# Kernel optimization log

Measured on AMD Instinct MI355X. Metric: run time of the kernel, lower is better.

## Reference

```python
import jax, jax.numpy as jnp
import numpy as np

NUM_LAYERS = 3


def setup_inputs() -> dict:
    key = jax.random.key(0)
    k1, k2, k3 = jax.random.split(key, 3)
    B, LT, LC, F = 16, 256, 768, 256
    batch_target = jax.random.normal(k1, (B, LT, F), dtype=jnp.float32)
    batch_claim = jax.random.normal(k2, (B, LC, F), dtype=jnp.float32)
    # adjacency is accepted but mathematically unused (original masked_fill is non-in-place and discarded)
    batch_adj = jax.random.randint(jax.random.fold_in(key, 7), (B, LT + LC, LT + LC), 0, 2, dtype=jnp.int32)
    # per-layer trans_linear weights, nn.Linear(F, F, bias=False): y = x @ W.T, W is [out, in]
    W_trans = jax.random.normal(k3, (NUM_LAYERS, F, F), dtype=jnp.float32) * (1.0 / np.sqrt(F))
    return {"batch_target": batch_target, "batch_claim": batch_claim, "batch_adj": batch_adj, "W_trans": W_trans}


def _gcn_layer(node_rep, W):
    # dot attention: score[b,i,j] = <h_i, h_j>  (symmetric all-pairs dot product)
    # NOTE: original's masked_fill(batch_adj == 0, -1e9) is NOT in-place and its
    # result is discarded, so no masking is applied -- reproduced faithfully here.
    corr = jnp.einsum('bif,bjf->bij', node_rep, node_rep)
    attn = jax.nn.softmax(corr, axis=2)              # softmax over j (dim=2)
    trans = jnp.einsum('blf,gf->blg', node_rep, W)   # trans_linear (bias=False)
    node_out = jax.nn.relu(node_rep + jnp.einsum('bij,bjf->bif', attn, trans))
    return node_out, attn


def reference(batch_target, batch_claim, batch_adj, W_trans):
    target_len = batch_target.shape[1]
    node_rep = jnp.concatenate([batch_target, batch_claim], axis=1)  # [B, L, F]
    all_node_rep, all_corr_score = (), ()
    for i in range(NUM_LAYERS):
        node_rep, corr_score = _gcn_layer(node_rep, W_trans[i])
        all_node_rep = all_node_rep + (node_rep,)
        all_corr_score = all_corr_score + (corr_score,)
        # gcn_dropout: identity in eval mode
    target_rep = node_rep[:, :target_len, :]
    claim_rep = node_rep[:, target_len:, :]
    return (target_rep, claim_rep, all_node_rep, all_corr_score)
```

## Files before the change

### kernel.cpp

```cpp
#include <hip/hip_runtime.h>

typedef _Float16 h16;
typedef _Float16 h16x8 __attribute__((ext_vector_type(8)));
typedef _Float16 h16x4 __attribute__((ext_vector_type(4)));
typedef float    f32x4 __attribute__((ext_vector_type(4)));

#define NBATCH 16
#define LROWS  1024
#define FDIM   256

#define OFF_TGT 0ull
#define OFF_CLM 1048576ull
#define OFF_NR  4194304ull
#define OFF_AT  16777216ull

__device__ __forceinline__ void split2(float x, h16& h, h16& l) {
    h = (h16)x;
    l = (h16)(x - (float)h);
}

typedef const __attribute__((address_space(1))) void gvoid;
typedef __attribute__((address_space(3))) void lvoid;
__device__ __forceinline__ void gl_lds16(const void* g, void* l) {
    __builtin_amdgcn_global_load_lds((gvoid*)g, (lvoid*)l, 16, 0, 0);
}

__device__ const unsigned char TRI_I[36] = {
    0,0,0,0,0,0,0,0, 1,1,1,1,1,1,1, 2,2,2,2,2,2, 3,3,3,3,3, 4,4,4,4, 5,5,5, 6,6, 7};
__device__ const unsigned char TRI_J[36] = {
    0,1,2,3,4,5,6,7, 1,2,3,4,5,6,7, 2,3,4,5,6,7, 3,4,5,6,7, 4,5,6,7, 5,6,7, 6,7, 7};

__global__ __launch_bounds__(256) void convert_all(const float* __restrict__ tgt,
                                                   const float* __restrict__ clm,
                                                   const float* __restrict__ W,
                                                   h16* __restrict__ xh, h16* __restrict__ xl,
                                                   h16* __restrict__ wh) {
    int bid = blockIdx.x;
    if (bid < 4096) {
        int b, i;
        if (bid < 2048) { b = bid & 7;       i = bid >> 3; }
        else            { b = 8 + (bid & 7); i = (bid - 2048) >> 3; }
        size_t e = ((size_t)b << 18) + (size_t)i * 1024 + (size_t)threadIdx.x * 4;
        int rf = (int)(e & 262143);
        int r  = rf >> 8, f = rf & 255;
        const float* src = (r < 256)
            ? tgt + ((size_t)b << 16) + ((size_t)r << 8) + f
            : clm + (size_t)b * 196608 + ((size_t)(r - 256) << 8) + f;
        f32x4 v = *(const f32x4*)src;
        h16x4 hv, lv;
#pragma unroll
        for (int j = 0; j < 4; ++j) { h16 hh, ll; split2(v[j], hh, ll); hv[j] = hh; lv[j] = ll; }
        *(h16x4*)(xh + e) = hv;
        *(h16x4*)(xl + e) = lv;
    } else {
        size_t e = ((size_t)(bid - 4096) * 256 + threadIdx.x) * 4;
        f32x4 v = *(const f32x4*)(W + e);
        h16x4 hv;
#pragma unroll
        for (int j = 0; j < 4; ++j) hv[j] = (h16)v[j];
        *(h16x4*)(wh + e) = hv;
    }
}

__global__ __launch_bounds__(256, 3) void gemm_ct(
    const h16* __restrict__ Xh, const h16* __restrict__ Xl,
    const h16* __restrict__ Wh,
    h16* __restrict__ Ptil, float2* __restrict__ part,
    h16* __restrict__ Th) {
    const int b = blockIdx.x & 15;
    const int u = blockIdx.x >> 4;
    const bool isCorr = u < 36;
    int it, jt;
    if (isCorr) { it = TRI_I[u]; jt = TRI_J[u]; }
    else        { int v = u - 36; it = v >> 1; jt = v & 1; }
    const int i0 = it * 128;
    const int j0 = jt * 128;
    const int t  = threadIdx.x;
    const int lane = t & 63, wid = t >> 6;
    const int wr = wid >> 1, wc = wid & 1;

    __shared__ alignas(16) char lds[32768];

    const size_t arow = ((size_t)b * LROWS + i0) * 256;
    const h16* bHp; const h16* bLp; size_t brow;
    if (isCorr) { bHp = Xh; bLp = Xl; brow = ((size_t)b * LROWS + j0) * 256; }
    else        { bHp = Wh; bLp = Xl; brow = (size_t)j0 * 256; }

    f32x4 acc[4][4];
#pragma unroll
    for (int i = 0; i < 4; ++i)
#pragma unroll
        for (int j = 0; j < 4; ++j) acc[i][j] = (f32x4){0.f, 0.f, 0.f, 0.f};

    const int grow = t >> 2;
    const int gq   = t & 3;

    for (int kt = 0; kt < 8; ++kt) {
        __syncthreads();
#pragma unroll
        for (int p = 0; p < 2; ++p) {
            int r = p * 64 + grow;
            size_t so = (size_t)r * 256 + kt * 32 + ((gq ^ ((r >> 1) & 3)) << 3);
            char* d = lds + p * 4096 + wid * 1024;
            gl_lds16(Xh + arow + so, d);
            gl_lds16(Xl + arow + so, d + 8192);
            gl_lds16(bHp + brow + so, d + 16384);
            if (isCorr) gl_lds16(bLp + brow + so, d + 24576);
        }
        __syncthreads();

        const int kq = lane >> 4;
        const int rA = wr * 64 + (lane & 15);
        const int rB = wc * 64 + (lane & 15);
        h16x8 ah[4], al[4], bh[4], bl[4];
#pragma unroll
        for (int mi = 0; mi < 4; ++mi) {
            int r   = rA + mi * 16;
            int off = r * 64 + ((kq ^ ((r >> 1) & 3)) << 4);
            ah[mi] = *(const h16x8*)(lds + off);
            al[mi] = *(const h16x8*)(lds + 8192 + off);
        }
#pragma unroll
        for (int nj = 0; nj < 4; ++nj) {
            int r   = rB + nj * 16;
            int off = r * 64 + ((kq ^ ((r >> 1) & 3)) << 4);
            bh[nj] = *(const h16x8*)(lds + 16384 + off);
            if (isCorr) bl[nj] = *(const h16x8*)(lds + 24576 + off);
        }
        __builtin_amdgcn_s_setprio(1);
#pragma unroll
        for (int mi = 0; mi < 4; ++mi)
#pragma unroll
            for (int nj = 0; nj < 4; ++nj) {
                acc[mi][nj] = __builtin_amdgcn_mfma_f32_16x16x32_f16(ah[mi], bh[nj], acc[mi][nj], 0, 0, 0);
                acc[mi][nj] = __builtin_amdgcn_mfma_f32_16x16x32_f16(al[mi], bh[nj], acc[mi][nj], 0, 0, 0);
                if (isCorr)
                    acc[mi][nj] = __builtin_amdgcn_mfma_f32_16x16x32_f16(ah[mi], bl[nj], acc[mi][nj], 0, 0, 0);
            }
        __builtin_amdgcn_s_setprio(0);
    }

    const int mBase = i0 + wr * 64;
    const int nBase = j0 + wc * 64;
    if (isCorr) {
        h16* Pb = Ptil + (size_t)b * LROWS * 1024;
        {
            const int chunk = jt * 2 + wc;
#pragma unroll
            for (int mi = 0; mi < 4; ++mi)
#pragma unroll
                for (int rg = 0; rg < 4; ++rg) {
                    float v0 = acc[mi][0][rg], v1 = acc[mi][1][rg];
                    float v2 = acc[mi][2][rg], v3 = acc[mi][3][rg];
                    float mx = fmaxf(fmaxf(v0, v1), fmaxf(v2, v3));
#pragma unroll
                    for (int off = 8; off >= 1; off >>= 1) mx = fmaxf(mx, __shfl_xor(mx, off, 64));
                    float e0 = __expf(v0 - mx), e1 = __expf(v1 - mx);
                    float e2 = __expf(v2 - mx), e3 = __expf(v3 - mx);
                    float s = e0 + e1 + e2 + e3;
#pragma unroll
                    for (int off = 8; off >= 1; off >>= 1) s += __shfl_xor(s, off, 64);
                    int row = mBase + mi * 16 + ((lane >> 4) * 4) + rg;
                    if ((lane & 15) == 0)
                        part[((size_t)b * 1024 + row) * 16 + chunk] = make_float2(mx, s);
                    size_t rb = (size_t)row * 1024 + nBase + (lane & 15);
                    Pb[rb]      = (h16)e0;
                    Pb[rb + 16] = (h16)e1;
                    Pb[rb + 32] = (h16)e2;
                    Pb[rb + 48] = (h16)e3;
                }
        }
        if (it != jt) {
            __syncthreads();
            const int chunk = it * 2 + wr;
            const int cl0 = wc * 64 + (lane & 15);
            const int r40 = wr * 64 + ((lane >> 4) << 2);
#pragma unroll
            for (int nj = 0; nj < 4; ++nj) {
                float mx = -3.0e38f;
#pragma unroll
                for (int mi = 0; mi < 4; ++mi)
#pragma unroll
                    for (int rg = 0; rg < 4; ++rg) mx = fmaxf(mx, acc[mi][nj][rg]);
                mx = fmaxf(mx, __shfl_xor(mx, 16, 64));
                mx = fmaxf(mx, __shfl_xor(mx, 32, 64));
                float s = 0.f;
                h16x4 pt[4];
#pragma unroll
                for (int mi = 0; mi < 4; ++mi)
#pragma unroll
                    for (int rg = 0; rg < 4; ++rg) {
                        float e = __expf(acc[mi][nj][rg] - mx);
                        s += e;
                        pt[mi][rg] = (h16)e;
                    }
                s += __shfl_xor(s, 16, 64);
                s += __shfl_xor(s, 32, 64);
                int n = nBase + nj * 16 + (lane & 15);
                if (lane < 16)
                    part[((size_t)b * 1024 + n) * 16 + chunk] = make_float2(mx, s);
                const int cl = cl0 + nj * 16;
#pragma unroll
                for (int mi = 0; mi < 4; ++mi) {
                    int r4 = r40 + mi * 16;
                    *(h16x4*)(lds + cl * 256 + (((r4 ^ ((cl & 7) << 2))) << 1)) = pt[mi];
                }
            }
            __syncthreads();
#pragma unroll
            for (int i8 = 0; i8 < 8; ++i8) {
                int cl = wid * 32 + i8 * 4 + (lane >> 4);
                int R  = (lane & 15) * 8;
                int k4 = (cl & 7) << 2;
                h16x4 v0 = *(const h16x4*)(lds + cl * 256 + (((R    ) ^ k4) << 1));
                h16x4 v1 = *(const h16x4*)(lds + cl * 256 + (((R + 4) ^ k4) << 1));
                h16x8 vv;
                vv[0] = v0[0]; vv[1] = v0[1]; vv[2] = v0[2]; vv[3] = v0[3];
                vv[4] = v1[0]; vv[5] = v1[1]; vv[6] = v1[2]; vv[7] = v1[3];
                *(h16x8*)(Pb + (size_t)(j0 + cl) * 1024 + i0 + R) = vv;
            }
        }
    } else {
#pragma unroll
        for (int mi = 0; mi < 4; ++mi)
#pragma unroll
            for (int nj = 0; nj < 4; ++nj) {
                int n  = nBase + nj * 16 + (lane & 15);
                int m0 = mBase + mi * 16 + ((lane >> 4) * 4);
                h16x4 hv;
#pragma unroll
                for (int rg = 0; rg < 4; ++rg) hv[rg] = (h16)acc[mi][nj][rg];
                size_t off = ((size_t)b * 256 + n) * 1024 + m0;
                *(h16x4*)(Th + off) = hv;
            }
    }
}

__global__ __launch_bounds__(256, 4) void gemm_pv(
    const h16* __restrict__ Ptil, const float2* __restrict__ part,
    float* __restrict__ At,
    const h16* __restrict__ Th,
    h16* __restrict__ Xh, h16* __restrict__ Xl,
    float* __restrict__ NodeOut, float* __restrict__ OutBase, int last) {
    const int id   = blockIdx.x;
    const int b    = (id & 7) | (((id >> 3) & 1) << 3);
    const int mt   = id >> 4;
    const int i0   = mt * 32;
    const int t    = threadIdx.x;
    const int lane = t & 63, wid = t >> 6;
    const int wc   = wid;

    __shared__ alignas(16) char lds[38912];
    float* sc = (float*)(lds + 36864);

    if (t < 32) {
        const float2* pp = part + ((size_t)b * 1024 + i0 + t) * 16;
        float2 v[16];
        float M = -3.0e38f;
#pragma unroll
        for (int c = 0; c < 16; ++c) { v[c] = pp[c]; M = fmaxf(M, v[c].x); }
        float S = 0.f;
#pragma unroll
        for (int c = 0; c < 16; ++c) S += v[c].y * __expf(v[c].x - M);
        float inv = 1.0f / S;
#pragma unroll
        for (int c = 0; c < 16; ++c) sc[t * 16 + c] = __expf(v[c].x - M) * inv;
    }
    __syncthreads();

    const h16* Prow = Ptil + ((size_t)b * LROWS + i0) * 1024;
    float* Arow = At + ((size_t)b * LROWS + i0) * 1024;
    const size_t tbase = (size_t)b * 256 * 1024;

    const int ar = t >> 3;
    const int ac = t & 7;

    f32x4 acc[2][4];
#pragma unroll
    for (int i = 0; i < 2; ++i)
#pragma unroll
        for (int j = 0; j < 4; ++j) acc[i][j] = (f32x4){0.f, 0.f, 0.f, 0.f};

    for (int kt = 0; kt < 16; ++kt) {
        h16x8 pt = *(const h16x8*)(Prow + (size_t)ar * 1024 + kt * 64 + ac * 8);
        float s  = sc[ar * 16 + kt];
        __syncthreads();

#pragma unroll
        for (int itr = 0; itr < 8; ++itr) {
            int g = itr * 32 + ar;
            size_t so = tbase + (size_t)g * 1024 + kt * 64 + ((ac ^ (g & 7)) << 3);
            char* d = lds + 4096 + itr * 4096 + wid * 1024;
            gl_lds16(Th + so, d);
        }

        f32x4 plo, phi;
#pragma unroll
        for (int e = 0; e < 4; ++e) plo[e] = (float)pt[e] * s;
#pragma unroll
        for (int e = 0; e < 4; ++e) phi[e] = (float)pt[4 + e] * s;
        *(f32x4*)(Arow + (size_t)ar * 1024 + kt * 64 + ac * 8)     = plo;
        *(f32x4*)(Arow + (size_t)ar * 1024 + kt * 64 + ac * 8 + 4) = phi;
        h16x8 a16;
#pragma unroll
        for (int e = 0; e < 4; ++e) { a16[e] = (h16)plo[e]; a16[4 + e] = (h16)phi[e]; }
        *(h16x8*)(lds + ar * 128 + ((ac ^ (ar & 7)) << 4)) = a16;
        __syncthreads();

        const int kq = lane >> 4;
        __builtin_amdgcn_s_setprio(1);
#pragma unroll
        for (int s2 = 0; s2 < 2; ++s2) {
            h16x8 ah[2], bh[4];
#pragma unroll
            for (int mi = 0; mi < 2; ++mi) {
                int r = mi * 16 + (lane & 15);
                ah[mi] = *(const h16x8*)(lds + r * 128 + (((s2 * 4 + kq) ^ (r & 7)) << 4));
            }
#pragma unroll
            for (int nf = 0; nf < 4; ++nf) {
                int g = wc * 64 + nf * 16 + (lane & 15);
                bh[nf] = *(const h16x8*)(lds + 4096 + g * 128 + (((s2 * 4 + kq) ^ (g & 7)) << 4));
            }
#pragma unroll
            for (int mi = 0; mi < 2; ++mi)
#pragma unroll
                for (int nf = 0; nf < 4; ++nf)
                    acc[mi][nf] = __builtin_amdgcn_mfma_f32_16x16x32_f16(ah[mi], bh[nf], acc[mi][nf], 0, 0, 0);
        }
        __builtin_amdgcn_s_setprio(0);
    }

#pragma unroll
    for (int mi = 0; mi < 2; ++mi)
#pragma unroll
        for (int nf = 0; nf < 4; ++nf) {
            int n = wc * 64 + nf * 16 + (lane & 15);
#pragma unroll
            for (int rg = 0; rg < 4; ++rg) {
                int m = i0 + mi * 16 + ((lane >> 4) * 4) + rg;
                size_t off = ((size_t)b * LROWS + m) * FDIM + n;
                float res = (float)Xh[off] + (float)Xl[off];
                float y   = res + acc[mi][nf][rg];
                y = y > 0.f ? y : 0.f;
                NodeOut[off] = y;
                h16 hh, ll; split2(y, hh, ll);
                Xh[off] = hh; Xl[off] = ll;
                if (last) {
                    float* dst = (m < 256)
                        ? OutBase + OFF_TGT + ((size_t)b << 16) + ((size_t)m << 8) + n
                        : OutBase + OFF_CLM + (size_t)b * 196608 + ((size_t)(m - 256) << 8) + n;
                    *dst = y;
                }
            }
        }
}

extern "C" void kernel_launch(void* const* d_in, const int* in_sizes, int n_in,
                              void* d_out, int out_size, void* d_ws, size_t ws_size,
                              hipStream_t stream) {
    (void)in_sizes; (void)n_in; (void)out_size; (void)ws_size;
    const float* tgt = (const float*)d_in[0];
    const float* clm = (const float*)d_in[1];
    const float* W   = (const float*)d_in[3];
    float* out = (float*)d_out;
    char*  ws  = (char*)d_ws;

    h16* xh = (h16*)(ws);
    h16* xl = (h16*)(ws + (8ull << 20));
    h16* th = (h16*)(ws + (16ull << 20));
    h16* wh = (h16*)(ws + (24ull << 20));
    float2* part = (float2*)(ws + (25ull << 20));
    h16* ptil = (h16*)(ws + (27ull << 20));

    convert_all<<<4288, 256, 0, stream>>>(tgt, clm, W, xh, xl, wh);

    for (int L = 0; L < 3; ++L) {
        float* at = out + OFF_AT + (size_t)L * 16777216ull;
        float* nr = out + OFF_NR + (size_t)L * 4194304ull;
        gemm_ct<<<832, 256, 0, stream>>>(xh, xl, wh + (size_t)L * 65536, ptil, part, th);
        gemm_pv<<<512, 256, 0, stream>>>(ptil, part, at, th, xh, xl, nr, out, L == 2);
    }
}
```

Before: 209.8 us.

## Stage softmax tiles through LDS for coalesced stores and skip duplicate diagonal loads

Diagonal correlation tiles now reuse the A-operand LDS buffers for the B operand instead of loading the same rows twice. The row-direction exp tile is staged in swizzled LDS and written to global memory as 16-byte vector stores rather than scattered 2-byte stores. The fp32 attention write in the PV kernel is merged into a single 8-wide vector store. The changes add extra barriers and LDS traffic in the epilogue in exchange for less global load and store traffic.

```diff
diff --git a/kernel.cpp b/kernel.cpp
--- a/kernel.cpp
+++ b/kernel.cpp
@@ -4,6 +4,7 @@
 typedef _Float16 h16x8 __attribute__((ext_vector_type(8)));
 typedef _Float16 h16x4 __attribute__((ext_vector_type(4)));
 typedef float    f32x4 __attribute__((ext_vector_type(4)));
+typedef float    f32x8 __attribute__((ext_vector_type(8)));
 
 #define NBATCH 16
 #define LROWS  1024
@@ -73,6 +74,7 @@
     int it, jt;
     if (isCorr) { it = TRI_I[u]; jt = TRI_J[u]; }
     else        { int v = u - 36; it = v >> 1; jt = v & 1; }
+    const bool diag = isCorr && (it == jt);
     const int i0 = it * 128;
     const int j0 = jt * 128;
     const int t  = threadIdx.x;
@@ -85,6 +87,9 @@
     const h16* bHp; const h16* bLp; size_t brow;
     if (isCorr) { bHp = Xh; bLp = Xl; brow = ((size_t)b * LROWS + j0) * 256; }
     else        { bHp = Wh; bLp = Xl; brow = (size_t)j0 * 256; }
+
+    const int bOffH = diag ? 0 : 16384;
+    const int bOffL = diag ? 8192 : 24576;
 
     f32x4 acc[4][4];
 #pragma unroll
@@ -104,8 +109,10 @@
             char* d = lds + p * 4096 + wid * 1024;
             gl_lds16(Xh + arow + so, d);
             gl_lds16(Xl + arow + so, d + 8192);
-            gl_lds16(bHp + brow + so, d + 16384);
-            if (isCorr) gl_lds16(bLp + brow + so, d + 24576);
+            if (!diag) {
+                gl_lds16(bHp + brow + so, d + 16384);
+                if (isCorr) gl_lds16(bLp + brow + so, d + 24576);
+            }
         }
         __syncthreads();
 
@@ -124,8 +131,8 @@
         for (int nj = 0; nj < 4; ++nj) {
             int r   = rB + nj * 16;
             int off = r * 64 + ((kq ^ ((r >> 1) & 3)) << 4);
-            bh[nj] = *(const h16x8*)(lds + 16384 + off);
-            if (isCorr) bl[nj] = *(const h16x8*)(lds + 24576 + off);
+            bh[nj] = *(const h16x8*)(lds + bOffH + off);
+            if (isCorr) bl[nj] = *(const h16x8*)(lds + bOffL + off);
         }
         __builtin_amdgcn_s_setprio(1);
 #pragma unroll
@@ -144,6 +151,7 @@
     const int nBase = j0 + wc * 64;
     if (isCorr) {
         h16* Pb = Ptil + (size_t)b * LROWS * 1024;
+        __syncthreads();
         {
             const int chunk = jt * 2 + wc;
 #pragma unroll
@@ -160,15 +168,25 @@
                     float s = e0 + e1 + e2 + e3;
 #pragma unroll
                     for (int off = 8; off >= 1; off >>= 1) s += __shfl_xor(s, off, 64);
-                    int row = mBase + mi * 16 + ((lane >> 4) * 4) + rg;
+                    int rl  = wr * 64 + mi * 16 + ((lane >> 4) * 4) + rg;
                     if ((lane & 15) == 0)
-                        part[((size_t)b * 1024 + row) * 16 + chunk] = make_float2(mx, s);
-                    size_t rb = (size_t)row * 1024 + nBase + (lane & 15);
-                    Pb[rb]      = (h16)e0;
-                    Pb[rb + 16] = (h16)e1;
-                    Pb[rb + 32] = (h16)e2;
-                    Pb[rb + 48] = (h16)e3;
+                        part[((size_t)b * 1024 + (i0 + rl)) * 16 + chunk] = make_float2(mx, s);
+                    int xr = ((rl >> 2) & 3) << 5;
+                    int c0 = wc * 64 + (lane & 15);
+                    *(h16*)(lds + rl * 256 + (((c0      ) * 2) ^ xr)) = (h16)e0;
+                    *(h16*)(lds + rl * 256 + (((c0 + 16) * 2) ^ xr)) = (h16)e1;
+                    *(h16*)(lds + rl * 256 + (((c0 + 32) * 2) ^ xr)) = (h16)e2;
+                    *(h16*)(lds + rl * 256 + (((c0 + 48) * 2) ^ xr)) = (h16)e3;
                 }
+        }
+        __syncthreads();
+#pragma unroll
+        for (int i8 = 0; i8 < 8; ++i8) {
+            int rl = wid * 32 + i8 * 4 + (lane >> 4);
+            int cb = (lane & 15) * 16;
+            int xr = ((rl >> 2) & 3) << 5;
+            h16x8 vv = *(const h16x8*)(lds + rl * 256 + (cb ^ xr));
+            *(h16x8*)(Pb + (size_t)(i0 + rl) * 1024 + j0 + (lane & 15) * 8) = vv;
         }
         if (it != jt) {
             __syncthreads();
@@ -294,16 +312,13 @@
             gl_lds16(Th + so, d);
         }
 
-        f32x4 plo, phi;
-#pragma unroll
-        for (int e = 0; e < 4; ++e) plo[e] = (float)pt[e] * s;
-#pragma unroll
-        for (int e = 0; e < 4; ++e) phi[e] = (float)pt[4 + e] * s;
-        *(f32x4*)(Arow + (size_t)ar * 1024 + kt * 64 + ac * 8)     = plo;
-        *(f32x4*)(Arow + (size_t)ar * 1024 + kt * 64 + ac * 8 + 4) = phi;
+        f32x8 pw;
+#pragma unroll
+        for (int e = 0; e < 8; ++e) pw[e] = (float)pt[e] * s;
+        *(f32x8*)(Arow + (size_t)ar * 1024 + kt * 64 + ac * 8) = pw;
         h16x8 a16;
 #pragma unroll
-        for (int e = 0; e < 4; ++e) { a16[e] = (h16)plo[e]; a16[4 + e] = (h16)phi[e]; }
+        for (int e = 0; e < 8; ++e) a16[e] = (h16)pw[e];
         *(h16x8*)(lds + ar * 128 + ((ac ^ (ar & 7)) << 4)) = a16;
         __syncthreads();
 
```

Measured after the change: 211.0 us. Within noise of the previous version (+0.6%).

## Reuse A tile for diagonal corr blocks, remap batch grid order, widen attn store

Applied to the files above, without the earlier changes.

Diagonal correlation tiles (it==jt) now skip loading the B operand and read B hi/lo from the already-loaded A tiles in LDS, which removes redundant global-to-LDS traffic. Both GEMM kernels remap blockIdx so the first half of the grid covers batches 0-7 and the second half batches 8-15, which changes which blocks run concurrently and may improve cache locality. The attention-row store is merged into one 8-float vector store. The remap assumes the grid sizes are exactly 832 and 512 blocks.

```diff
diff --git a/kernel.cpp b/kernel.cpp
--- a/kernel.cpp
+++ b/kernel.cpp
@@ -4,6 +4,7 @@
 typedef _Float16 h16x8 __attribute__((ext_vector_type(8)));
 typedef _Float16 h16x4 __attribute__((ext_vector_type(4)));
 typedef float    f32x4 __attribute__((ext_vector_type(4)));
+typedef float    f32x8 __attribute__((ext_vector_type(8)));
 
 #define NBATCH 16
 #define LROWS  1024
@@ -67,12 +68,14 @@
     const h16* __restrict__ Wh,
     h16* __restrict__ Ptil, float2* __restrict__ part,
     h16* __restrict__ Th) {
-    const int b = blockIdx.x & 15;
-    const int u = blockIdx.x >> 4;
+    int b, u;
+    if (blockIdx.x < 416) { b = blockIdx.x & 7;               u = blockIdx.x >> 3; }
+    else                  { b = 8 + ((blockIdx.x - 416) & 7); u = (blockIdx.x - 416) >> 3; }
     const bool isCorr = u < 36;
     int it, jt;
     if (isCorr) { it = TRI_I[u]; jt = TRI_J[u]; }
     else        { int v = u - 36; it = v >> 1; jt = v & 1; }
+    const bool diag = isCorr && (it == jt);
     const int i0 = it * 128;
     const int j0 = jt * 128;
     const int t  = threadIdx.x;
@@ -85,6 +88,9 @@
     const h16* bHp; const h16* bLp; size_t brow;
     if (isCorr) { bHp = Xh; bLp = Xl; brow = ((size_t)b * LROWS + j0) * 256; }
     else        { bHp = Wh; bLp = Xl; brow = (size_t)j0 * 256; }
+
+    const int bOffH = diag ? 0 : 16384;
+    const int bOffL = diag ? 8192 : 24576;
 
     f32x4 acc[4][4];
 #pragma unroll
@@ -104,8 +110,10 @@
             char* d = lds + p * 4096 + wid * 1024;
             gl_lds16(Xh + arow + so, d);
             gl_lds16(Xl + arow + so, d + 8192);
-            gl_lds16(bHp + brow + so, d + 16384);
-            if (isCorr) gl_lds16(bLp + brow + so, d + 24576);
+            if (!diag) {
+                gl_lds16(bHp + brow + so, d + 16384);
+                if (isCorr) gl_lds16(bLp + brow + so, d + 24576);
+            }
         }
         __syncthreads();
 
@@ -124,8 +132,8 @@
         for (int nj = 0; nj < 4; ++nj) {
             int r   = rB + nj * 16;
             int off = r * 64 + ((kq ^ ((r >> 1) & 3)) << 4);
-            bh[nj] = *(const h16x8*)(lds + 16384 + off);
-            if (isCorr) bl[nj] = *(const h16x8*)(lds + 24576 + off);
+            bh[nj] = *(const h16x8*)(lds + bOffH + off);
+            if (isCorr) bl[nj] = *(const h16x8*)(lds + bOffL + off);
         }
         __builtin_amdgcn_s_setprio(1);
 #pragma unroll
@@ -243,8 +251,9 @@
     h16* __restrict__ Xh, h16* __restrict__ Xl,
     float* __restrict__ NodeOut, float* __restrict__ OutBase, int last) {
     const int id   = blockIdx.x;
-    const int b    = (id & 7) | (((id >> 3) & 1) << 3);
-    const int mt   = id >> 4;
+    int b, mt;
+    if (id < 256) { b = id & 7;               mt = id >> 3; }
+    else          { b = 8 + ((id - 256) & 7); mt = (id - 256) >> 3; }
     const int i0   = mt * 32;
     const int t    = threadIdx.x;
     const int lane = t & 63, wid = t >> 6;
@@ -294,16 +303,13 @@
             gl_lds16(Th + so, d);
         }
 
-        f32x4 plo, phi;
-#pragma unroll
-        for (int e = 0; e < 4; ++e) plo[e] = (float)pt[e] * s;
-#pragma unroll
-        for (int e = 0; e < 4; ++e) phi[e] = (float)pt[4 + e] * s;
-        *(f32x4*)(Arow + (size_t)ar * 1024 + kt * 64 + ac * 8)     = plo;
-        *(f32x4*)(Arow + (size_t)ar * 1024 + kt * 64 + ac * 8 + 4) = phi;
+        f32x8 pw;
+#pragma unroll
+        for (int e = 0; e < 8; ++e) pw[e] = (float)pt[e] * s;
+        *(f32x8*)(Arow + (size_t)ar * 1024 + kt * 64 + ac * 8) = pw;
         h16x8 a16;
 #pragma unroll
-        for (int e = 0; e < 4; ++e) { a16[e] = (h16)plo[e]; a16[4 + e] = (h16)phi[e]; }
+        for (int e = 0; e < 8; ++e) a16[e] = (h16)pw[e];
         *(h16x8*)(lds + ar * 128 + ((ac ^ (ar & 7)) << 4)) = a16;
         __syncthreads();
 
```

Result: slower. 217.2 us (median of 2 runs) (+3.5%).
